# Performance work log

Hardware: AMD Instinct MI355X
Metric: run time of the kernel (lower is better)

Reference implementation:

```python
import jax, jax.numpy as jnp
import numpy as np
from jax import lax

H = W = 128            # feature map spatial size (2h x 2w)
WIN = 16               # attention window size
DIM = 512
HEADS = 8
DIM_HEAD = 64
INNER = HEADS * DIM_HEAD
SCALE = DIM_HEAD ** -0.5
KEEP = 44
IOU_T = 0.2

_s = np.arange(0, H - WIN + 1, WIN // 2)
_sx, _sy = np.meshgrid(_s, _s)
WINDOWS = np.stack([_sx.ravel(), _sy.ravel(), _sx.ravel() + WIN - 1, _sy.ravel() + WIN - 1], 1).astype(np.float32)
M = WINDOWS.shape[0]   # 225
SX = jnp.asarray(WINDOWS[:, 0].astype(np.int32))
SY = jnp.asarray(WINDOWS[:, 1].astype(np.int32))

# ---- static pairwise IoU (torchvision convention: area=(x2-x1)*(y2-y1)) ----
_x1, _y1, _x2, _y2 = WINDOWS[:, 0], WINDOWS[:, 1], WINDOWS[:, 2], WINDOWS[:, 3]
_area = (_x2 - _x1) * (_y2 - _y1)
_iw = np.clip(np.minimum(_x2[:, None], _x2[None]) - np.maximum(_x1[:, None], _x1[None]), 0, None)
_ih = np.clip(np.minimum(_y2[:, None], _y2[None]) - np.maximum(_y1[:, None], _y1[None]), 0, None)
_inter = _iw * _ih
IOU = jnp.asarray((_inter / (_area[:, None] + _area[None] - _inter)).astype(np.float32))

# ---- roi_align (aligned=False, 1 sample/bin) == separable bilinear resample ----
_bin = (WIN - 1.0) / WIN
_r = (np.arange(WIN) + 0.5) * _bin
_q = np.floor(_r).astype(int)
_f = _r - _q
_A = np.zeros((WIN, WIN), np.float32)
_A[np.arange(WIN), _q] = 1.0 - _f
_A[np.arange(WIN), np.minimum(_q + 1, WIN - 1)] += _f
BILIN = jnp.asarray(_A)


def _nms_select(score):
    """Greedy NMS over the static window set; return first KEEP kept indices."""
    order = jnp.argsort(-score)
    iou_s = IOU[order][:, order]
    def body(i, supp):
        return supp | ((~supp[i]) & (iou_s[i] > IOU_T) & (jnp.arange(M) > i))
    supp = lax.fori_loop(0, M, body, jnp.zeros((M,), dtype=bool))
    pos = jnp.where(~supp, jnp.arange(M), M)
    pos = jnp.minimum(jnp.sort(pos)[:KEEP], M - 1)
    return order[pos]


def setup_inputs() -> dict:
    key = jax.random.key(0)
    k1, k2, k3, k4 = jax.random.split(key, 4)
    x = jax.random.normal(k1, (8, H * W, DIM), dtype=jnp.float32)
    prob = jax.random.uniform(k2, (8, 4, H // 2, W // 2), dtype=jnp.float32)
    W_fix = jnp.ones((1, 1, WIN // 2, WIN // 2), jnp.float32)   # FixCNN ones kernel
    W_qkv = jax.random.normal(k3, (3 * INNER, DIM), jnp.float32) * 0.02
    W_out = jax.random.normal(k4, (DIM, INNER), jnp.float32) * 0.02
    b_out = jnp.zeros((DIM,), jnp.float32)
    return {"x": x, "prob": prob, "W_fix": W_fix, "W_qkv": W_qkv, "W_out": W_out, "b_out": b_out}


def reference(x, prob, W_fix, W_qkv, W_out, b_out):
    b = x.shape[0]
    # entropy over class channels
    entropy = -jnp.sum(prob * jnp.log2(prob + 1e-10), axis=1)           # (b, 64, 64)
    # FixCNN: ones 8x8 kernel, stride 4, then /64
    score = lax.conv(entropy[:, None], W_fix, (WIN // 4, WIN // 4), 'VALID')
    score = (score / float((WIN // 2) ** 2)).reshape(b, -1)             # (b, M)
    x2d = x.transpose(0, 2, 1).reshape(b, DIM, H, W)                    # b d h w
    rng = jnp.arange(WIN)

    def per_batch(feat, sc):
        idx = _nms_select(sc)                                           # (KEEP,)
        sy, sx = SY[idx], SX[idx]
        # gather integer 16x16 patches (box corners are integers)
        patches = jax.vmap(lambda y, xc: lax.dynamic_slice(feat, (0, y, xc), (DIM, WIN, WIN)))(sy, sx)
        # roi_align bilinear resample (separable)
        pat = jnp.einsum('pi,mdij,qj->mdpq', BILIN, patches, BILIN)     # (KEEP, d, 16, 16)
        xi = pat.transpose(0, 2, 3, 1).reshape(KEEP, WIN * WIN, DIM)    # m n d
        qkv = xi @ W_qkv.T
        q, k, v = jnp.split(qkv, 3, axis=-1)
        to_h = lambda t: t.reshape(KEEP, WIN * WIN, HEADS, DIM_HEAD).transpose(0, 2, 1, 3)
        q, k, v = to_h(q), to_h(k), to_h(v)
        attn = jax.nn.softmax(jnp.einsum('mhnd,mhkd->mhnk', q, k) * SCALE, axis=-1)
        out = jnp.einsum('mhnk,mhkd->mhnd', attn, v)
        out = out.transpose(0, 2, 1, 3).reshape(KEEP, WIN * WIN, INNER)
        out = out @ W_out.T + b_out                                     # (KEEP, n, DIM)
        out2d = out.reshape(KEEP, WIN, WIN, DIM).transpose(0, 3, 1, 2)  # m d h w
        yy = sy[:, None, None] + rng[None, :, None]                     # (KEEP,16,1)
        xx = sx[:, None, None] + rng[None, None, :]                     # (KEEP,1,16)
        acc = jnp.zeros((DIM, H, W), x.dtype).at[:, yy, xx].add(out2d.transpose(1, 0, 2, 3))
        cnt = jnp.zeros((H, W), x.dtype).at[yy, xx].add(1.0)
        return acc, cnt

    acc, cnt = jax.vmap(per_batch)(x2d, score)
    outx = (acc / (cnt[:, None] + 1e-10)).reshape(b, DIM, H * W).transpose(0, 2, 1)
    return x + outx
```

## Files before the change

### kernel.cpp

```cpp
#include <hip/hip_runtime.h>
#include <type_traits>
#include <utility>

typedef unsigned short u16;
typedef __attribute__((ext_vector_type(8))) short short8;
typedef __attribute__((ext_vector_type(8))) __bf16 bf16v8;
typedef __attribute__((ext_vector_type(4))) float f32x4;
typedef __attribute__((ext_vector_type(16))) float f32x16;

template <typename T, typename = void> struct mfma_ok : std::false_type {};
template <typename T>
struct mfma_ok<T, std::void_t<decltype(__builtin_amdgcn_mfma_f32_16x16x32_bf16(
    std::declval<T>(), std::declval<T>(), std::declval<f32x4>(), 0, 0, 0))>>
    : std::true_type {};
using frag8 = std::conditional_t<mfma_ok<bf16v8>::value, bf16v8, short8>;

#define MFMA16(a, b, c) __builtin_amdgcn_mfma_f32_16x16x32_bf16((a), (b), (c), 0, 0, 0)
#define MFMA32(a, b, c) __builtin_amdgcn_mfma_f32_32x32x16_bf16((a), (b), (c), 0, 0, 0)

__device__ __forceinline__ float bf2f(u16 u) {
  unsigned v = ((unsigned)u) << 16;
  return __builtin_bit_cast(float, v);
}
__device__ __forceinline__ u16 f2bf(float f) {
  unsigned u = __builtin_bit_cast(unsigned, f);
  u = (u + 0x7fffu + ((u >> 16) & 1u)) >> 16;
  return (u16)u;
}
__device__ __forceinline__ unsigned cvtpk_bf16(float lo, float hi) {
  unsigned r;
  asm("v_cvt_pk_bf16_f32 %0, %1, %2" : "=v"(r) : "v"(lo), "v"(hi));
  return r;
}
__device__ __forceinline__ void gl16(const u16* g, u16* l) {
  __builtin_amdgcn_global_load_lds((__attribute__((address_space(1))) void*)(g),
                                   (__attribute__((address_space(3))) void*)(l), 16, 0, 0);
}
__device__ __forceinline__ void vmw8() { asm volatile("s_waitcnt vmcnt(8)" ::: "memory"); }
__device__ __forceinline__ void vmw0() { asm volatile("s_waitcnt vmcnt(0)" ::: "memory"); }
__device__ __forceinline__ void lgw0() { asm volatile("s_waitcnt lgkmcnt(0)" ::: "memory"); }

__global__ void k_score(const float* __restrict__ prob, const float* __restrict__ wfix,
                        float* __restrict__ scores) {
  const int b = blockIdx.x, tid = threadIdx.x;
  __shared__ float ent[64 * 64];
  __shared__ float wf[64];
  if (tid < 64) wf[tid] = wfix[tid];
  const float* pb = prob + (size_t)b * 4 * 4096;
  for (int p = tid; p < 4096; p += 256) {
    float e = 0.f;
#pragma unroll
    for (int ch = 0; ch < 4; ++ch) {
      float v = pb[ch * 4096 + p];
      e -= v * log2f(v + 1e-10f);
    }
    ent[p] = e;
  }
  __syncthreads();
  if (tid < 225) {
    int wy = tid / 15, wx = tid % 15;
    float s = 0.f;
    for (int a = 0; a < 8; ++a)
      for (int c = 0; c < 8; ++c)
        s += ent[(wy * 4 + a) * 64 + wx * 4 + c] * wf[a * 8 + c];
    scores[b * 225 + tid] = s * (1.0f / 64.0f);
  }
}

__device__ __forceinline__ float iou_pair(int wa, int wb) {
  float x1a = (float)((wa % 15) * 8), y1a = (float)((wa / 15) * 8);
  float x1b = (float)((wb % 15) * 8), y1b = (float)((wb / 15) * 8);
  float iw = fminf(x1a, x1b) + 15.f - fmaxf(x1a, x1b);
  float ih = fminf(y1a, y1b) + 15.f - fmaxf(y1a, y1b);
  iw = fmaxf(iw, 0.f);
  ih = fmaxf(ih, 0.f);
  float inter = iw * ih;
  return inter / (450.f - inter);
}

__global__ void k_nms(const float* __restrict__ scores, int* __restrict__ sel,
                      int* __restrict__ kept, float* __restrict__ mult) {
  const int b = blockIdx.x, t = threadIdx.x;
  __shared__ float s[225];
  __shared__ int order[225];
  __shared__ unsigned char supp[225];
  __shared__ int idx44[44];
  __shared__ int ks[225];
  __shared__ float ml[225];
  if (t < 225) s[t] = scores[b * 225 + t];
  __syncthreads();
  if (t < 225) {
    float st = s[t];
    int r = 0;
    for (int j = 0; j < 225; ++j) {
      float sj = s[j];
      r += (sj > st) || (sj == st && j < t);
    }
    order[r] = t;
    supp[t] = 0;
    ks[t] = -1;
    ml[t] = 0.f;
  }
  __syncthreads();
  for (int i = 0; i < 224; ++i) {
    if (t > i && t < 225 && !supp[i]) {
      if (iou_pair(order[i], order[t]) > 0.2f) supp[t] = 1;
    }
    __syncthreads();
  }
  if (t == 0) {
    int k = 0;
    for (int i = 0; i < 225 && k < 44; ++i)
      if (!supp[i]) idx44[k++] = order[i];
    while (k < 44) idx44[k++] = order[224];
    for (int k2 = 0; k2 < 44; ++k2) {
      int w = idx44[k2];
      if (ks[w] < 0) ks[w] = k2;
      ml[w] += 1.f;
    }
  }
  __syncthreads();
  if (t < 225) {
    kept[b * 225 + t] = ks[t];
    mult[b * 225 + t] = ml[t];
  }
  if (t < 44) sel[b * 44 + t] = idx44[t];
}

__global__ void k_castw(const float* __restrict__ Wq, const float* __restrict__ Wo,
                        u16* __restrict__ wqb, u16* __restrict__ wob) {
  int idx = blockIdx.x * 256 + threadIdx.x;
  if (idx < 786432) wqb[idx] = f2bf(Wq[idx]);
  int i2 = idx - 786432;
  if (i2 >= 0 && i2 < 262144) wob[i2] = f2bf(Wo[i2]);
}

__global__ __launch_bounds__(256) void k_gather(const float* __restrict__ x,
                                                const int* __restrict__ sel,
                                                u16* __restrict__ xi) {
  const size_t idx = (size_t)blockIdx.x * 256 + threadIdx.x;
  const int dc = (int)(idx & 63);
  const int pq = (int)((idx >> 6) & 255);
  const int g = (int)(idx >> 14);
  const int b = g / 44;
  const int w = sel[g];
  const int sy = (w / 15) * 8, sx = (w % 15) * 8;
  const int p = pq >> 4, q = pq & 15;
  float rp = ((float)p + 0.5f) * 0.9375f;
  int i0 = (int)rp;
  float fp = rp - (float)i0;
  float rq = ((float)q + 0.5f) * 0.9375f;
  int j0 = (int)rq;
  float fq = rq - (float)j0;
  const float w00 = (1.f - fp) * (1.f - fq), w01 = (1.f - fp) * fq;
  const float w10 = fp * (1.f - fq), w11 = fp * fq;
  const float* xb = x + ((size_t)b * 16384 + (size_t)(sy + i0) * 128 + sx + j0) * 512 + dc * 8;
  const float4* t00 = (const float4*)xb;
  const float4* t01 = (const float4*)(xb + 512);
  const float4* t10 = (const float4*)(xb + 512 * 128);
  const float4* t11 = (const float4*)(xb + 512 * 129);
  float acc[8];
#pragma unroll
  for (int h = 0; h < 2; ++h) {
    float4 a = t00[h], bb = t01[h], c = t10[h], d = t11[h];
    acc[h * 4 + 0] = w00 * a.x + w01 * bb.x + w10 * c.x + w11 * d.x;
    acc[h * 4 + 1] = w00 * a.y + w01 * bb.y + w10 * c.y + w11 * d.y;
    acc[h * 4 + 2] = w00 * a.z + w01 * bb.z + w10 * c.z + w11 * d.z;
    acc[h * 4 + 3] = w00 * a.w + w01 * bb.w + w10 * c.w + w11 * d.w;
  }
  short8 o;
#pragma unroll
  for (int e = 0; e < 8; ++e) o[e] = (short)f2bf(acc[e]);
  *(short8*)&xi[((size_t)g * 256 + pq) * 512 + dc * 8] = o;
}

template <int BIAS>
__global__ __launch_bounds__(512, 2) void k_gemm256(const u16* __restrict__ A,
                                                    const u16* __restrict__ B, u16* __restrict__ C,
                                                    const float* __restrict__ bias, int M, int N,
                                                    int K, int nbn) {
  __shared__ u16 sA[2][256 * 64];
  __shared__ u16 sB[2][256 * 64];
  const int tid = threadIdx.x, lane = tid & 63, wv = tid >> 6;
  const int f = blockIdx.x;
  const int q8 = gridDim.x >> 3;
  const int wg = (f & 7) * q8 + (f >> 3);
  const int bm = wg / nbn, bn = wg % nbn;
  const int wm = (wv >> 2) * 128, wn = (wv & 3) * 64;
  const int l15 = lane & 15, k8 = (lane >> 4) * 8;
  const int xorv = (l15 & 7) * 8;
  const int srow = tid >> 3;
  const int sc8 = ((tid ^ (tid >> 3)) & 7) * 8;
  const u16* Ab = A + (size_t)(bm * 256 + srow) * K + sc8;
  const u16* Bb = B + (size_t)(bn * 256 + srow) * K + sc8;

  f32x4 acc[8][4] = {};

#define STAGE(kt, buf)                                                       \
  {                                                                          \
    const int ko = (kt) * 64;                                                \
    _Pragma("unroll") for (int c = 0; c < 4; ++c) {                          \
      gl16(Ab + (size_t)(c * 64) * K + ko, &sA[buf][c * 4096 + wv * 512]);   \
      gl16(Bb + (size_t)(c * 64) * K + ko, &sB[buf][c * 4096 + wv * 512]);   \
    }                                                                        \
  }

  STAGE(0, 0);
  STAGE(1, 1);

  for (int t = 0; t < 8; ++t) {
    const int buf = t & 1;
    if (t == 7)
      vmw0();
    else
      vmw8();
    __builtin_amdgcn_sched_barrier(0);
    __builtin_amdgcn_s_barrier();
#pragma unroll
    for (int mh = 0; mh < 2; ++mh) {
      frag8 af[4][2], bf[2][2][2];
#pragma unroll
      for (int i = 0; i < 4; ++i)
#pragma unroll
        for (int kk = 0; kk < 2; ++kk)
          af[i][kk] = *(const frag8*)&sA[buf][(wm + (mh * 4 + i) * 16 + l15) * 64 +
                                             ((kk * 32 + k8) ^ xorv)];
#pragma unroll
      for (int nh = 0; nh < 2; ++nh)
#pragma unroll
        for (int j = 0; j < 2; ++j)
#pragma unroll
          for (int kk = 0; kk < 2; ++kk)
            bf[nh][j][kk] = *(const frag8*)&sB[buf][(wn + (nh * 2 + j) * 16 + l15) * 64 +
                                                    ((kk * 32 + k8) ^ xorv)];
      lgw0();
      __builtin_amdgcn_sched_barrier(0);
      __builtin_amdgcn_s_setprio(1);
#pragma unroll
      for (int nh = 0; nh < 2; ++nh)
#pragma unroll
        for (int i = 0; i < 4; ++i)
#pragma unroll
          for (int j = 0; j < 2; ++j)
#pragma unroll
            for (int kk = 0; kk < 2; ++kk)
              acc[mh * 4 + i][nh * 2 + j] =
                  MFMA16(af[i][kk], bf[nh][j][kk], acc[mh * 4 + i][nh * 2 + j]);
      __builtin_amdgcn_s_setprio(0);
    }
    __builtin_amdgcn_s_barrier();
    if (t < 6) STAGE(t + 2, buf);
  }
#undef STAGE

  const int cc = lane & 15, rr = (lane >> 4) * 4;
#pragma unroll
  for (int i = 0; i < 8; ++i)
#pragma unroll
    for (int j = 0; j < 4; ++j) {
      int col = bn * 256 + wn + j * 16 + cc;
      float badd = BIAS ? bias[col] : 0.f;
#pragma unroll
      for (int e = 0; e < 4; ++e) {
        int row = bm * 256 + wm + i * 16 + rr + e;
        C[(size_t)row * N + col] = f2bf(acc[i][j][e] + badd);
      }
    }
}

__global__ __launch_bounds__(256, 3) void k_attn(const u16* __restrict__ qkv,
                                                 u16* __restrict__ aout) {
  const int g = blockIdx.x;
  const int win = g >> 3, h = g & 7;
  const int tid = threadIdx.x, lane = tid & 63, wv = tid >> 6;
  const int l31 = lane & 31, l5 = lane >> 5;
  __shared__ u16 smem[17664];
  u16* KbB = smem;
  u16* VtB = smem + 8704;
  const u16* base = qkv + (size_t)win * 256 * 1536;
  const u16* kbase = base + 512 + h * 64;
  const u16* vbase = base + 1024 + h * 64;
  const int prow = tid >> 2, pc16 = (tid & 3) * 16;

  frag8 qf[2][4];
#pragma unroll
  for (int qt = 0; qt < 2; ++qt)
#pragma unroll
    for (int c = 0; c < 4; ++c)
      qf[qt][c] = *(const frag8*)(base + (size_t)(wv * 64 + qt * 32 + l31) * 1536 + h * 64 +
                                  c * 16 + l5 * 8);
  {
    const u16* kp = kbase + (size_t)prow * 1536 + pc16;
    short8 ka = *(const short8*)kp;
    short8 kb2 = *(const short8*)(kp + 8);
    const u16* vp = vbase + (size_t)prow * 1536 + pc16;
    short8 va = *(const short8*)vp;
    short8 vb2 = *(const short8*)(vp + 8);
    *(short8*)&KbB[prow * 68 + pc16] = ka;
    *(short8*)&KbB[prow * 68 + pc16 + 8] = kb2;
#pragma unroll
    for (int e = 0; e < 8; ++e) {
      VtB[(pc16 + e) * 70 + prow] = (u16)va[e];
      VtB[(pc16 + 8 + e) * 70 + prow] = (u16)vb2[e];
    }
  }
  __syncthreads();

  f32x16 of[2][2] = {};
  float m_run[2] = {-3e38f, -3e38f};
  float l_run[2] = {0.f, 0.f};

  int cur = 0;
  for (int kb = 0; kb < 4; ++kb) {
    short8 pk0 = {}, pk1 = {}, pv0 = {}, pv1 = {};
    if (kb < 3) {
      const u16* kp = kbase + (size_t)((kb + 1) * 64 + prow) * 1536 + pc16;
      pk0 = *(const short8*)kp;
      pk1 = *(const short8*)(kp + 8);
      const u16* vp = vbase + (size_t)((kb + 1) * 64 + prow) * 1536 + pc16;
      pv0 = *(const short8*)vp;
      pv1 = *(const short8*)(vp + 8);
    }
#pragma unroll
    for (int qt = 0; qt < 2; ++qt) {
      f32x16 s0 = {}, s1 = {};
#pragma unroll
      for (int c = 0; c < 4; ++c) {
        frag8 kf0 = *(const frag8*)&KbB[cur * 4352 + l31 * 68 + c * 16 + l5 * 8];
        frag8 kf1 = *(const frag8*)&KbB[cur * 4352 + (32 + l31) * 68 + c * 16 + l5 * 8];
        s0 = MFMA32(kf0, qf[qt][c], s0);
        s1 = MFMA32(kf1, qf[qt][c], s1);
      }
      float tm[16];
#pragma unroll
      for (int r = 0; r < 16; ++r) tm[r] = fmaxf(s0[r], s1[r]);
#pragma unroll
      for (int r = 0; r < 8; ++r) tm[r] = fmaxf(tm[r], tm[r + 8]);
#pragma unroll
      for (int r = 0; r < 4; ++r) tm[r] = fmaxf(tm[r], tm[r + 4]);
      float pm = fmaxf(fmaxf(tm[0], tm[1]), fmaxf(tm[2], tm[3]));
      pm = fmaxf(pm, __shfl_xor(pm, 32));
      if (!__all(pm <= m_run[qt] + 64.f)) {
        float mn = fmaxf(m_run[qt], pm);
        float corr = __expf((m_run[qt] - mn) * 0.125f);
        l_run[qt] *= corr;
#pragma unroll
        for (int dt = 0; dt < 2; ++dt)
#pragma unroll
          for (int r = 0; r < 16; ++r) of[qt][dt][r] *= corr;
        m_run[qt] = mn;
      }
      const float mqt = m_run[qt];
      float ls = 0.f;
#pragma unroll
      for (int kt = 0; kt < 2; ++kt) {
        const f32x16 sv = kt ? s1 : s0;
        float p[16];
#pragma unroll
        for (int r = 0; r < 16; ++r) p[r] = __expf((sv[r] - mqt) * 0.125f);
        float e0 = (p[0] + p[1]) + (p[2] + p[3]);
        float e1 = (p[4] + p[5]) + (p[6] + p[7]);
        float e2 = (p[8] + p[9]) + (p[10] + p[11]);
        float e3 = (p[12] + p[13]) + (p[14] + p[15]);
        ls += (e0 + e1) + (e2 + e3);
#pragma unroll
        for (int cc = 0; cc < 2; ++cc) {
          const int bx = cc * 8;
          unsigned a0 = cvtpk_bf16(p[bx + 0], p[bx + 1]);
          unsigned a1 = cvtpk_bf16(p[bx + 2], p[bx + 3]);
          unsigned b0 = cvtpk_bf16(p[bx + 4], p[bx + 5]);
          unsigned b1 = cvtpk_bf16(p[bx + 6], p[bx + 7]);
          asm("v_permlane32_swap_b32 %0, %1" : "+v"(a0), "+v"(b0));
          asm("v_permlane32_swap_b32 %0, %1" : "+v"(a1), "+v"(b1));
          uint4 fu;
          fu.x = a0;
          fu.y = a1;
          fu.z = b0;
          fu.w = b1;
          frag8 pb = __builtin_bit_cast(frag8, fu);
#pragma unroll
          for (int dt = 0; dt < 2; ++dt) {
            frag8 va = *(const frag8*)&VtB[cur * 4480 + (dt * 32 + l31) * 70 + kt * 32 + cc * 16 +
                                           l5 * 8];
            of[qt][dt] = MFMA32(va, pb, of[qt][dt]);
          }
        }
      }
      l_run[qt] += ls;
    }
    if (kb < 3) {
      *(short8*)&KbB[(cur ^ 1) * 4352 + prow * 68 + pc16] = pk0;
      *(short8*)&KbB[(cur ^ 1) * 4352 + prow * 68 + pc16 + 8] = pk1;
      u16* vd = &VtB[(cur ^ 1) * 4480 + prow];
#pragma unroll
      for (int e = 0; e < 8; ++e) {
        vd[(pc16 + e) * 70] = (u16)pv0[e];
        vd[(pc16 + 8 + e) * 70] = (u16)pv1[e];
      }
    }
    __syncthreads();
    cur ^= 1;
  }

  float inv[2];
#pragma unroll
  for (int qt = 0; qt < 2; ++qt) {
    float lt = l_run[qt] + __shfl_xor(l_run[qt], 32);
    inv[qt] = 1.0f / lt;
  }
  u16* sc = smem + wv * 4352;
  __syncthreads();
#pragma unroll
  for (int qt = 0; qt < 2; ++qt)
#pragma unroll
    for (int dt = 0; dt < 2; ++dt)
#pragma unroll
      for (int j = 0; j < 4; ++j) {
        unsigned w0 = cvtpk_bf16(of[qt][dt][4 * j + 0] * inv[qt], of[qt][dt][4 * j + 1] * inv[qt]);
        unsigned w1 = cvtpk_bf16(of[qt][dt][4 * j + 2] * inv[qt], of[qt][dt][4 * j + 3] * inv[qt]);
        *(uint2*)&sc[(qt * 32 + l31) * 68 + dt * 32 + 8 * j + 4 * l5] = make_uint2(w0, w1);
      }
  asm volatile("" ::: "memory");
#pragma unroll
  for (int rep = 0; rep < 8; ++rep) {
    int row = rep * 8 + (lane >> 3);
    uint2 lo = *(const uint2*)&sc[row * 68 + (lane & 7) * 8];
    uint2 hi = *(const uint2*)&sc[row * 68 + (lane & 7) * 8 + 4];
    *(int4*)&aout[(size_t)(win * 256 + wv * 64 + row) * 512 + h * 64 + (lane & 7) * 8] =
        make_int4((int)lo.x, (int)lo.y, (int)hi.x, (int)hi.y);
  }
}

__global__ void k_final(const float* __restrict__ x, const u16* __restrict__ proj,
                        const int* __restrict__ kept, const float* __restrict__ mult,
                        float* __restrict__ out) {
  const size_t idx = (size_t)blockIdx.x * 256 + threadIdx.x;
  const int dci = (int)(idx & 31);
  const int pix = (int)((idx >> 5) & 16383);
  const int b = (int)(idx >> 19);
  const int y = pix >> 7, xc = pix & 127;
  float acc[16];
#pragma unroll
  for (int e = 0; e < 16; ++e) acc[e] = 0.f;
  float c = 0.f;
  const int wyh = y >> 3, wxh = xc >> 3;
#pragma unroll
  for (int a = 0; a < 2; ++a) {
    int wy = wyh - 1 + a;
    if (wy < 0 || wy > 14) continue;
#pragma unroll
    for (int bb = 0; bb < 2; ++bb) {
      int wx = wxh - 1 + bb;
      if (wx < 0 || wx > 14) continue;
      int w = wy * 15 + wx;
      int slot = kept[b * 225 + w];
      if (slot < 0) continue;
      float ml = mult[b * 225 + w];
      c += ml;
      const u16* pr = proj +
                      ((size_t)((b * 44 + slot) * 256 + (y - wy * 8) * 16 + (xc - wx * 8))) * 512 +
                      (size_t)dci * 16;
      short8 v0 = *(const short8*)pr;
      short8 v1 = *(const short8*)(pr + 8);
#pragma unroll
      for (int e = 0; e < 8; ++e) acc[e] += ml * bf2f((u16)v0[e]);
#pragma unroll
      for (int e = 0; e < 8; ++e) acc[8 + e] += ml * bf2f((u16)v1[e]);
    }
  }
  const float inv = 1.f / (c + 1e-10f);
  const size_t off = ((size_t)(b * 16384 + pix)) * 512 + (size_t)dci * 16;
  const float4* xp = (const float4*)(x + off);
  float4* op = (float4*)(out + off);
#pragma unroll
  for (int q4 = 0; q4 < 4; ++q4) {
    float4 xv = xp[q4];
    float4 ov;
    ov.x = xv.x + acc[q4 * 4 + 0] * inv;
    ov.y = xv.y + acc[q4 * 4 + 1] * inv;
    ov.z = xv.z + acc[q4 * 4 + 2] * inv;
    ov.w = xv.w + acc[q4 * 4 + 3] * inv;
    op[q4] = ov;
  }
}

extern "C" void kernel_launch(void* const* d_in, const int* in_sizes, int n_in, void* d_out,
                              int out_size, void* d_ws, size_t ws_size, hipStream_t stream) {
  const float* x = (const float*)d_in[0];
  const float* prob = (const float*)d_in[1];
  const float* wfix = (const float*)d_in[2];
  const float* Wq = (const float*)d_in[3];
  const float* Wo = (const float*)d_in[4];
  const float* bo = (const float*)d_in[5];
  float* out = (float*)d_out;
  char* ws = (char*)d_ws;

  float* scores = (float*)(ws + 0);
  int* sel = (int*)(ws + 8192);
  int* kept = (int*)(ws + 16384);
  float* mult = (float*)(ws + 24576);
  u16* wqb = (u16*)(ws + 32768);
  u16* wob = (u16*)(ws + 32768 + 1572864);
  u16* xi = (u16*)(ws + 4194304);
  u16* qkv = (u16*)(ws + 4194304 + 92274688);
  u16* aout = xi;
  u16* proj = qkv;

  k_score<<<8, 256, 0, stream>>>(prob, wfix, scores);
  k_nms<<<8, 256, 0, stream>>>(scores, sel, kept, mult);
  k_castw<<<4096, 256, 0, stream>>>(Wq, Wo, wqb, wob);
  k_gather<<<22528, 256, 0, stream>>>(x, sel, xi);
  k_gemm256<0><<<2112, 512, 0, stream>>>(xi, wqb, qkv, nullptr, 90112, 1536, 512, 6);
  k_attn<<<2816, 256, 0, stream>>>(qkv, aout);
  k_gemm256<1><<<704, 512, 0, stream>>>(aout, wob, proj, bo, 90112, 512, 512, 2);
  k_final<<<16384, 256, 0, stream>>>(x, proj, kept, mult, out);
}
```

Measured before the change: 734.9 us.

## Load K fragments directly from global and stage full transposed V once

```diff
diff --git a/kernel.cpp b/kernel.cpp
--- a/kernel.cpp
+++ b/kernel.cpp
@@ -268,20 +268,27 @@
     }
 }
 
-__global__ __launch_bounds__(256, 3) void k_attn(const u16* __restrict__ qkv,
+__global__ __launch_bounds__(256, 4) void k_attn(const u16* __restrict__ qkv,
                                                  u16* __restrict__ aout) {
   const int g = blockIdx.x;
   const int win = g >> 3, h = g & 7;
   const int tid = threadIdx.x, lane = tid & 63, wv = tid >> 6;
   const int l31 = lane & 31, l5 = lane >> 5;
-  __shared__ u16 smem[17664];
-  u16* KbB = smem;
-  u16* VtB = smem + 8704;
+  __shared__ u16 smem[17408];
+  u16* VtB = smem;
   const u16* base = qkv + (size_t)win * 256 * 1536;
   const u16* kbase = base + 512 + h * 64;
   const u16* vbase = base + 1024 + h * 64;
-  const int prow = tid >> 2, pc16 = (tid & 3) * 16;
-
+
+  {
+    const u16* vp = vbase + (size_t)tid * 1536;
+#pragma unroll
+    for (int c8 = 0; c8 < 64; c8 += 8) {
+      short8 v = *(const short8*)(vp + c8);
+#pragma unroll
+      for (int e2 = 0; e2 < 8; ++e2) VtB[(c8 + e2) * 258 + tid] = (u16)v[e2];
+    }
+  }
   frag8 qf[2][4];
 #pragma unroll
   for (int qt = 0; qt < 2; ++qt)
@@ -289,47 +296,27 @@
     for (int c = 0; c < 4; ++c)
       qf[qt][c] = *(const frag8*)(base + (size_t)(wv * 64 + qt * 32 + l31) * 1536 + h * 64 +
                                   c * 16 + l5 * 8);
-  {
-    const u16* kp = kbase + (size_t)prow * 1536 + pc16;
-    short8 ka = *(const short8*)kp;
-    short8 kb2 = *(const short8*)(kp + 8);
-    const u16* vp = vbase + (size_t)prow * 1536 + pc16;
-    short8 va = *(const short8*)vp;
-    short8 vb2 = *(const short8*)(vp + 8);
-    *(short8*)&KbB[prow * 68 + pc16] = ka;
-    *(short8*)&KbB[prow * 68 + pc16 + 8] = kb2;
-#pragma unroll
-    for (int e = 0; e < 8; ++e) {
-      VtB[(pc16 + e) * 70 + prow] = (u16)va[e];
-      VtB[(pc16 + 8 + e) * 70 + prow] = (u16)vb2[e];
-    }
-  }
   __syncthreads();
 
   f32x16 of[2][2] = {};
   float m_run[2] = {-3e38f, -3e38f};
   float l_run[2] = {0.f, 0.f};
 
-  int cur = 0;
   for (int kb = 0; kb < 4; ++kb) {
-    short8 pk0 = {}, pk1 = {}, pv0 = {}, pv1 = {};
-    if (kb < 3) {
-      const u16* kp = kbase + (size_t)((kb + 1) * 64 + prow) * 1536 + pc16;
-      pk0 = *(const short8*)kp;
-      pk1 = *(const short8*)(kp + 8);
-      const u16* vp = vbase + (size_t)((kb + 1) * 64 + prow) * 1536 + pc16;
-      pv0 = *(const short8*)vp;
-      pv1 = *(const short8*)(vp + 8);
-    }
+    frag8 kf[2][4];
+#pragma unroll
+    for (int kr = 0; kr < 2; ++kr)
+#pragma unroll
+      for (int c = 0; c < 4; ++c)
+        kf[kr][c] = *(const frag8*)(kbase + (size_t)(kb * 64 + kr * 32 + l31) * 1536 + c * 16 +
+                                    l5 * 8);
 #pragma unroll
     for (int qt = 0; qt < 2; ++qt) {
       f32x16 s0 = {}, s1 = {};
 #pragma unroll
       for (int c = 0; c < 4; ++c) {
-        frag8 kf0 = *(const frag8*)&KbB[cur * 4352 + l31 * 68 + c * 16 + l5 * 8];
-        frag8 kf1 = *(const frag8*)&KbB[cur * 4352 + (32 + l31) * 68 + c * 16 + l5 * 8];
-        s0 = MFMA32(kf0, qf[qt][c], s0);
-        s1 = MFMA32(kf1, qf[qt][c], s1);
+        s0 = MFMA32(kf[0][c], qf[qt][c], s0);
+        s1 = MFMA32(kf[1][c], qf[qt][c], s1);
       }
       float tm[16];
 #pragma unroll
@@ -380,7 +367,7 @@
           frag8 pb = __builtin_bit_cast(frag8, fu);
 #pragma unroll
           for (int dt = 0; dt < 2; ++dt) {
-            frag8 va = *(const frag8*)&VtB[cur * 4480 + (dt * 32 + l31) * 70 + kt * 32 + cc * 16 +
+            frag8 va = *(const frag8*)&VtB[(dt * 32 + l31) * 258 + kb * 64 + kt * 32 + cc * 16 +
                                            l5 * 8];
             of[qt][dt] = MFMA32(va, pb, of[qt][dt]);
           }
@@ -388,18 +375,6 @@
       }
       l_run[qt] += ls;
     }
-    if (kb < 3) {
-      *(short8*)&KbB[(cur ^ 1) * 4352 + prow * 68 + pc16] = pk0;
-      *(short8*)&KbB[(cur ^ 1) * 4352 + prow * 68 + pc16 + 8] = pk1;
-      u16* vd = &VtB[(cur ^ 1) * 4480 + prow];
-#pragma unroll
-      for (int e = 0; e < 8; ++e) {
-        vd[(pc16 + e) * 70] = (u16)pv0[e];
-        vd[(pc16 + 8 + e) * 70] = (u16)pv1[e];
-      }
-    }
-    __syncthreads();
-    cur ^= 1;
   }
 
   float inv[2];
```

New measurement: 1.118 ms. 52.1% more time.
